# Kernel optimization log

Hardware: AMD Instinct MI355X
Metric: run time of the kernel (lower is better)

## Reference

```python
import jax, jax.numpy as jnp
import numpy as np

V = 32          # num_variables
T = 48          # num_time_bins
D = 512         # d_model
H = 8           # num_heads
HD = D // H     # head_dim = 64
OD = 16         # observation_dim
B = 4


def setup_inputs() -> dict:
    key = jax.random.key(0)
    ks = jax.random.split(key, 20)
    s = 0.02
    inp = {
        'h': jax.random.normal(ks[0], (B, T, V, D), jnp.float32),
        'observation_state': jax.random.normal(ks[1], (B, T, V, 2), jnp.float32),
        'Wq': jax.random.normal(ks[2], (D, D), jnp.float32) * s,
        'bq': jnp.zeros((D,), jnp.float32),
        'Wk': jax.random.normal(ks[3], (D, D), jnp.float32) * s,
        'bk': jnp.zeros((D,), jnp.float32),
        'Wv': jax.random.normal(ks[4], (D, D), jnp.float32) * s,
        'bv': jnp.zeros((D,), jnp.float32),
        'Wo': jax.random.normal(ks[5], (D, D), jnp.float32) * s,
        'bo': jnp.zeros((D,), jnp.float32),
        'Woq': jax.random.normal(ks[6], (2, H * OD), jnp.float32) * 0.5,
        'boq': jnp.zeros((H * OD,), jnp.float32),
        'Wok': jax.random.normal(ks[7], (2, H * OD), jnp.float32) * 0.5,
        'bok': jnp.zeros((H * OD,), jnp.float32),
        'variable_bias': jax.random.normal(ks[8], (H, V, V), jnp.float32) * 0.01,
        'relative_time_bias': jax.random.normal(ks[9], (H, 2 * T - 1), jnp.float32) * 0.01,
    }
    return inp


def reference(h, observation_state, Wq, bq, Wk, bk, Wv, bv, Wo, bo,
              Woq, boq, Wok, bok, variable_bias, relative_time_bias):
    N = T * V
    scale = 1.0 / np.sqrt(HD)
    obs_scale = 1.0 / np.sqrt(OD)

    # static index buffers (constants)
    flat_var_ids = jnp.tile(jnp.arange(V), T)                       # [N]
    flat_time_ids = jnp.repeat(jnp.arange(T), V)                    # [N]
    rel_index = flat_time_ids[:, None] - flat_time_ids[None, :] + (T - 1)  # [N,N]

    fh = h.reshape(B, N, D)
    fo = observation_state.reshape(B, N, 2)

    def heads(x, nh, hd):
        return x.reshape(B, N, nh, hd).transpose(0, 2, 1, 3)  # [B,H,N,hd]

    q = heads(fh @ Wq + bq, H, HD)
    k = heads(fh @ Wk + bk, H, HD)
    v = heads(fh @ Wv + bv, H, HD)
    oq = heads(fo @ Woq + boq, H, OD)
    ok = heads(fo @ Wok + bok, H, OD)

    content = jnp.einsum('bhnd,bhmd->bhnm', q, k) * scale
    obs = jnp.einsum('bhnd,bhmd->bhnm', oq, ok) * obs_scale
    var_scores = variable_bias[:, flat_var_ids[:, None], flat_var_ids[None, :]]  # [H,N,N]
    time_scores = relative_time_bias[:, rel_index]                                # [H,N,N]

    scores = content + obs + var_scores[None] + time_scores[None]
    attn = jax.nn.softmax(scores, axis=-1)  # dropout off (inference)
    out = jnp.einsum('bhnm,bhmd->bhnd', attn, v)
    out = out.transpose(0, 2, 1, 3).reshape(B, N, D)
    out = out @ Wo + bo
    return out.reshape(B, T, V, D)
```

## Files before the change

kernel.cpp:

```cpp
#include <hip/hip_runtime.h>
#include <math.h>

typedef __bf16 bf16x8 __attribute__((ext_vector_type(8)));
typedef float f32x4 __attribute__((ext_vector_type(4)));
typedef short short4v __attribute__((ext_vector_type(4)));
typedef short short8v __attribute__((ext_vector_type(8)));

#define NB 4
#define NT 48
#define NV 32
#define ND 512
#define NH 8
#define NN 1536
#define NBN 6144
#define L2E 1.44269504f

#define GLOAD_LDS(g, l) \
    __builtin_amdgcn_global_load_lds( \
        (const __attribute__((address_space(1))) void*)(g), \
        (__attribute__((address_space(3))) void*)(l), 16, 0, 0)

__global__ __launch_bounds__(256) void prep(
    const float* __restrict__ h, const float* __restrict__ obs,
    const float* __restrict__ Wq, const float* __restrict__ Wk,
    const float* __restrict__ Wv, const float* __restrict__ Wo,
    const float* __restrict__ bq, const float* __restrict__ bk,
    const float* __restrict__ bv,
    const float* __restrict__ Wok, const float* __restrict__ bok,
    __bf16* __restrict__ h_bf, __bf16* __restrict__ WcatT,
    __bf16* __restrict__ WoT, float* __restrict__ biascat,
    __bf16* __restrict__ kx)
{
    __shared__ float ts[64][68];
    const int tid = threadIdx.x;
    const int bx = blockIdx.x;
    if (bx < 1536) {
        int t = bx * 256 + tid;
        const float4* src = (const float4*)h + (size_t)t * 2;
        float4 a = src[0], b = src[1];
        __bf16 r[8] = {(__bf16)a.x, (__bf16)a.y, (__bf16)a.z, (__bf16)a.w,
                       (__bf16)b.x, (__bf16)b.y, (__bf16)b.z, (__bf16)b.w};
        *(uint4*)(h_bf + (size_t)t * 8) = *(uint4*)r;
    } else if (bx < 1792) {
        int bw = bx - 1536;
        const int p = bw >> 6, tile = bw & 63;
        const int k0 = (tile >> 3) * 64, c0 = (tile & 7) * 64;
        const float* W = (p == 0) ? Wq : (p == 1) ? Wk : (p == 2) ? Wv : Wo;
        const float scale = (p == 0) ? 0.125f * L2E : 1.0f;
        #pragma unroll
        for (int i = 0; i < 4; i++) {
            int r = (tid >> 4) + i * 16;
            float4 v = *(const float4*)(W + (size_t)(k0 + r) * 512 + c0 + (tid & 15) * 4);
            *(float4*)&ts[r][(tid & 15) * 4] = v;
        }
        __syncthreads();
        __bf16 tmp[16];
        #pragma unroll
        for (int j = 0; j < 16; j++)
            tmp[j] = (__bf16)(ts[(tid & 3) * 16 + j][tid >> 2] * scale);
        int crow = c0 + (tid >> 2);
        __bf16* dst = (p < 3)
            ? WcatT + ((size_t)(p * 512 + crow)) * 512 + k0 + (tid & 3) * 16
            : WoT   + ((size_t)crow) * 512 + k0 + (tid & 3) * 16;
        *(uint4*)dst = *(uint4*)tmp;
        *(uint4*)(dst + 8) = *(uint4*)(tmp + 8);
        if (p < 3 && k0 == 0 && tid < 64) {
            const float* bb = (p == 0) ? bq : (p == 1) ? bk : bv;
            biascat[p * 512 + c0 + tid] = bb[c0 + tid] * scale;
        }
    } else {
        int t = (bx - 1792) * 256 + tid;
        int row = t >> 1, half = t & 1;
        __bf16* dst = kx + (size_t)row * 96 + 64 + half * 16;
        if (half == 0) {
            int bh = row / NN, n = row - bh * NN;
            int b = bh >> 3, hh = bh & 7;
            size_t bn = (size_t)b * NN + n;
            float o0 = obs[bn * 2], o1 = obs[bn * 2 + 1];
            int f = hh * 16;
            __bf16 tmp[16];
            #pragma unroll
            for (int j = 0; j < 16; j++)
                tmp[j] = (__bf16)(o0 * Wok[f + j] + o1 * Wok[128 + f + j] + bok[f + j]);
            *(uint4*)dst       = *(uint4*)tmp;
            *(uint4*)(dst + 8) = *(uint4*)(tmp + 8);
        } else {
            uint4 z = {0, 0, 0, 0};
            *(uint4*)dst       = z;
            *(uint4*)(dst + 8) = z;
        }
    }
}

template<int TM, bool BF16OUT>
__global__ __launch_bounds__(256) void gemm_mfma(
    const __bf16* __restrict__ A, const __bf16* __restrict__ Bt,
    const float* __restrict__ bias, float* __restrict__ Cf,
    __bf16* __restrict__ qarr, __bf16* __restrict__ kx,
    __bf16* __restrict__ vt)
{
    constexpr int MT = TM / 32;
    __shared__ __align__(16) char smem[34816];
    char* const As0 = smem;
    char* const As1 = smem + TM * 64;
    char* const Bs0 = smem + TM * 128;
    char* const Bs1 = smem + TM * 128 + 8192;
    const int tid = threadIdx.x;
    const int w = tid >> 6, lane = tid & 63;
    const int quad = lane >> 4, l16 = lane & 15;
    const int wm = w >> 1, wn = w & 1;
    const int n0 = blockIdx.x * 128, m0 = blockIdx.y * TM;

    const int sm = tid >> 2;
    const int sk = ((tid & 3) ^ ((sm >> 1) & 3)) * 8;
    const __bf16* aptr = A  + (size_t)(m0 + sm) * 512 + sk;
    const __bf16* bptr = Bt + (size_t)(n0 + sm) * 512 + sk;

    f32x4 zero4 = {0.f, 0.f, 0.f, 0.f};
    f32x4 acc[MT][4];
    #pragma unroll
    for (int i = 0; i < MT; i++)
        #pragma unroll
        for (int j = 0; j < 4; j++) acc[i][j] = zero4;

    auto STAGE = [&](char* dA, char* dB, int kt) {
        GLOAD_LDS(aptr + kt, dA + tid * 16);
        if (TM == 128) GLOAD_LDS(aptr + 64 * 512 + kt, dA + 4096 + tid * 16);
        GLOAD_LDS(bptr + kt, dB + tid * 16);
        GLOAD_LDS(bptr + 64 * 512 + kt, dB + 4096 + tid * 16);
    };
    auto COMPUTE = [&](const char* Asb, const char* Bsb) {
        bf16x8 af[MT], bfr[4];
        #pragma unroll
        for (int mt = 0; mt < MT; mt++) {
            int rr = wm * (TM / 2) + mt * 16 + l16;
            af[mt] = *(const bf16x8*)(Asb + rr * 64 + (quad ^ ((rr >> 1) & 3)) * 16);
        }
        #pragma unroll
        for (int nt = 0; nt < 4; nt++) {
            int rr = wn * 64 + nt * 16 + l16;
            bfr[nt] = *(const bf16x8*)(Bsb + rr * 64 + (quad ^ ((rr >> 1) & 3)) * 16);
        }
        #pragma unroll
        for (int mt = 0; mt < MT; mt++)
            #pragma unroll
            for (int nt = 0; nt < 4; nt++)
                acc[mt][nt] = __builtin_amdgcn_mfma_f32_16x16x32_bf16(
                    af[mt], bfr[nt], acc[mt][nt], 0, 0, 0);
    };

    STAGE(As0, Bs0, 0);
    asm volatile("s_waitcnt vmcnt(0)" ::: "memory");
    __builtin_amdgcn_s_barrier();
    for (int kt = 0; kt < 512; kt += 64) {
        STAGE(As1, Bs1, kt + 32);
        COMPUTE(As0, Bs0);
        asm volatile("s_waitcnt vmcnt(0)" ::: "memory");
        __builtin_amdgcn_s_barrier();
        if (kt + 64 < 512) STAGE(As0, Bs0, kt + 64);
        COMPUTE(As1, Bs1);
        asm volatile("s_waitcnt vmcnt(0)" ::: "memory");
        __builtin_amdgcn_s_barrier();
    }

    __syncthreads();
    if (BF16OUT) {
        if (n0 >= 1024) {
            __bf16* CsT = (__bf16*)smem;
            #pragma unroll
            for (int nt = 0; nt < 4; nt++) {
                int cl = wn * 64 + nt * 16 + l16;
                float bia = bias[n0 + cl];
                #pragma unroll
                for (int mt = 0; mt < MT; mt++) {
                    int rl0 = wm * (TM / 2) + mt * 16 + quad * 4;
                    __bf16 pk[4];
                    #pragma unroll
                    for (int r = 0; r < 4; r++)
                        pk[r] = (__bf16)(acc[mt][nt][r] + bia);
                    *(uint2*)&CsT[cl * 136 + rl0] = *(uint2*)pk;
                }
            }
            __syncthreads();
            int cl = tid >> 1, half = tid & 1;
            int f0 = (n0 + cl) & 511;
            int hh = f0 >> 6, d = f0 & 63;
            int dt = d >> 4, l16v = d & 15;
            int bidx = m0 / NN, nm = m0 - bidx * NN;
            int bh = bidx * 8 + hh;
            int mtv = (nm >> 6) + half;
            #pragma unroll
            for (int j = 0; j < 8; j++) {
                uint4 v = *(uint4*)&CsT[cl * 136 + half * 64 + j * 8];
                __bf16* pp = (__bf16*)&v;
                int q0 = (j & 1) * 2;
                size_t fo = ((size_t)(bh * 24 + mtv) * 8 + (j >> 1) * 2 + (dt >> 1)) * 512
                            + (dt & 1) * 4 + l16v * 8;
                *(uint2*)(vt + fo + q0 * 128)       = *(uint2*)&pp[0];
                *(uint2*)(vt + fo + (q0 + 1) * 128) = *(uint2*)&pp[4];
            }
        } else {
            __bf16* Cs = (__bf16*)smem;
            #pragma unroll
            for (int mt = 0; mt < MT; mt++)
                #pragma unroll
                for (int nt = 0; nt < 4; nt++) {
                    int cl = wn * 64 + nt * 16 + l16;
                    float bia = bias[n0 + cl];
                    #pragma unroll
                    for (int r = 0; r < 4; r++) {
                        int rl = wm * (TM / 2) + mt * 16 + quad * 4 + r;
                        Cs[rl * 132 + cl] = (__bf16)(acc[mt][nt][r] + bia);
                    }
                }
            __syncthreads();
            int rl = tid >> 1, hb = tid & 1;
            int grow = m0 + rl;
            int col0 = n0 + hb * 64;
            int p = col0 >> 9, f0 = col0 & 511, hh = f0 >> 6;
            int bidx = grow / NN, n = grow - bidx * NN;
            __bf16* dst = (p == 0) ? qarr + (size_t)grow * 512 + f0
                                   : kx + ((size_t)(bidx * 8 + hh) * NN + n) * 96;
            #pragma unroll
            for (int j = 0; j < 8; j++) {
                uint2 lo = *(uint2*)&Cs[rl * 132 + hb * 64 + j * 8];
                uint2 hi = *(uint2*)&Cs[rl * 132 + hb * 64 + j * 8 + 4];
                uint4 v = {lo.x, lo.y, hi.x, hi.y};
                *(uint4*)(dst + j * 8) = v;
            }
        }
    } else {
        float* Csf = (float*)smem;
        #pragma unroll
        for (int mt = 0; mt < MT; mt++)
            #pragma unroll
            for (int nt = 0; nt < 4; nt++) {
                int cl = wn * 64 + nt * 16 + l16;
                float bia = bias[n0 + cl];
                #pragma unroll
                for (int r = 0; r < 4; r++) {
                    int rl = wm * (TM / 2) + mt * 16 + quad * 4 + r;
                    Csf[rl * 132 + cl] = acc[mt][nt][r] + bia;
                }
            }
        __syncthreads();
        int rl = tid >> 2, q4 = tid & 3;
        float* dst = Cf + (size_t)(m0 + rl) * 512 + n0 + q4 * 32;
        #pragma unroll
        for (int j = 0; j < 8; j++) {
            uint4 v = *(uint4*)&Csf[rl * 132 + q4 * 32 + j * 4];
            *(uint4*)(dst + j * 4) = v;
        }
    }
}

__global__ __launch_bounds__(256, 3) void attn_mfma(
    const __bf16* __restrict__ qarr, const __bf16* __restrict__ kx,
    const __bf16* __restrict__ vt, const float* __restrict__ obs,
    const float* __restrict__ Woq, const float* __restrict__ boq,
    const float* __restrict__ varb, const float* __restrict__ rtb,
    __bf16* __restrict__ aout)
{
    __shared__ __align__(16) __bf16 Ks[2][64][128];
    __shared__ float rts[96];

    const int tid = threadIdx.x;
    const int w = tid >> 6, lane = tid & 63;
    const int quad = lane >> 4, l16 = lane & 15;
    const int bh = blockIdx.x, qt = blockIdx.y;
    const int b = bh >> 3, h = bh & 7;
    const int n0 = qt * 64;

    if (tid < 95) rts[tid] = rtb[h * 95 + tid] * L2E;

    const int ck = (tid & 15) ^ ((tid >> 4) & 7);
    const __bf16* kbase = kx + (size_t)bh * NN * 96 + ck * 8;
    auto STAGE_K = [&](int p, int m0s) {
        #pragma unroll
        for (int i = 0; i < 4; i++) {
            int row = i * 16 + (tid >> 4);
            GLOAD_LDS(kbase + (size_t)(m0s + row) * 96,
                      (char*)Ks + p * 16384 + i * 4096 + tid * 16);
        }
    };
    STAGE_K(0, 0);
    STAGE_K(1, 64);

    const __bf16* vwb = vt + (size_t)bh * 24 * 4096 + lane * 8;

    const int nl = w * 16 + l16;
    const size_t qrow = (size_t)(b * NN + n0 + nl);
    bf16x8 bq_[3];
    bq_[0] = *(const bf16x8*)(qarr + qrow * 512 + h * 64 + quad * 8);
    bq_[1] = *(const bf16x8*)(qarr + qrow * 512 + h * 64 + 32 + quad * 8);
    {
        uint4 a2u = {0u, 0u, 0u, 0u};
        if (quad < 2) {
            float o0 = obs[qrow * 2], o1 = obs[qrow * 2 + 1];
            int f = h * 16 + quad * 8;
            const float sc = 0.25f * L2E;
            __bf16 tmp[8];
            #pragma unroll
            for (int j = 0; j < 8; j++)
                tmp[j] = (__bf16)(sc * (o0 * Woq[f + j] + o1 * Woq[128 + f + j]
                                        + boq[f + j]));
            a2u = *(uint4*)tmp;
        }
        bq_[2] = *(bf16x8*)&a2u;
    }

    const int rm = (w & 1) * 16 + l16;
    float4 vbA = *(const float4*)(varb + h * 1024 + rm * 32 + quad * 4);
    float4 vbB = *(const float4*)(varb + h * 1024 + rm * 32 + 16 + quad * 4);
    float vA[4] = {vbA.x * L2E, vbA.y * L2E, vbA.z * L2E, vbA.w * L2E};
    float vB[4] = {vbB.x * L2E, vbB.y * L2E, vbB.z * L2E, vbB.w * L2E};
    const int tn = 2 * qt + (w >> 1);

    union { __bf16 e[4]; short4v s; } one_u;
    #pragma unroll
    for (int j = 0; j < 4; j++) one_u.e[j] = (__bf16)1.0f;
    const short4v ones = one_u.s;

    f32x4 zero4 = {0.f, 0.f, 0.f, 0.f};
    f32x4 o_p[4];
    f32x4 lpa = zero4;
    #pragma unroll
    for (int i = 0; i < 4; i++) o_p[i] = zero4;

    auto QK = [&](int p, f32x4* sc) {
        __builtin_amdgcn_s_setprio(1);
        #pragma unroll
        for (int ct = 0; ct < 4; ct++) {
            f32x4 d = zero4;
            int row = ct * 16 + l16;
            #pragma unroll
            for (int ks = 0; ks < 3; ks++) {
                bf16x8 kf = *(const bf16x8*)((const char*)Ks + p * 16384
                                + row * 256 + (((ks * 4 + quad) ^ (row & 7)) * 16));
                d = __builtin_amdgcn_mfma_f32_16x16x32_bf16(kf, bq_[ks], d, 0, 0, 0);
            }
            sc[ct] = d;
        }
        __builtin_amdgcn_s_setprio(0);
    };
    auto SM = [&](const f32x4* sc, int mt, short4v* pf) {
        float tb0 = rts[tn - 2 * mt + 47];
        float tb1 = rts[tn - 2 * mt + 46];
        #pragma unroll
        for (int ct = 0; ct < 4; ct++) {
            float tb = (ct & 2) ? tb1 : tb0;
            const float* vv = (ct & 1) ? vB : vA;
            union { __bf16 e[4]; short4v s; } pk;
            #pragma unroll
            for (int r = 0; r < 4; r++)
                pk.e[r] = (__bf16)exp2f(sc[ct][r] + tb + vv[r]);
            pf[ct] = pk.s;
        }
    };
    auto PV = [&](const short8v* vfr, const short4v* pf) {
        __builtin_amdgcn_s_setprio(1);
        #pragma unroll
        for (int ct = 0; ct < 4; ct++) {
            lpa = __builtin_amdgcn_mfma_f32_16x16x16bf16_1k(ones, pf[ct], lpa, 0, 0, 0);
            #pragma unroll
            for (int dt = 0; dt < 4; dt++) {
                short8v v8 = vfr[ct * 2 + (dt >> 1)];
                short4v va = (dt & 1)
                    ? __builtin_shufflevector(v8, v8, 4, 5, 6, 7)
                    : __builtin_shufflevector(v8, v8, 0, 1, 2, 3);
                o_p[dt] = __builtin_amdgcn_mfma_f32_16x16x16bf16_1k(
                    va, pf[ct], o_p[dt], 0, 0, 0);
            }
        }
        __builtin_amdgcn_s_setprio(0);
    };

    __syncthreads();

    for (int i = 0; i < 12; i++) {
        const int mt0 = 2 * i;
        short8v v0[8];
        {
            const __bf16* vp = vwb + (size_t)mt0 * 4096;
            #pragma unroll
            for (int fi = 0; fi < 8; fi++)
                v0[fi] = *(const short8v*)(vp + fi * 512);
        }
        f32x4 sc0[4], sc1[4];
        QK(0, sc0);
        QK(1, sc1);
        __syncthreads();
        if (i < 11) {
            STAGE_K(0, (mt0 + 2) * 64);
            STAGE_K(1, (mt0 + 3) * 64);
        }
        short4v p0[4];
        SM(sc0, mt0, p0);
        short8v v1[8];
        {
            const __bf16* vp = vwb + (size_t)(mt0 + 1) * 4096;
            #pragma unroll
            for (int fi = 0; fi < 8; fi++)
                v1[fi] = *(const short8v*)(vp + fi * 512);
        }
        PV(v0, p0);
        short4v p1[4];
        SM(sc1, mt0 + 1, p1);
        PV(v1, p1);
        __syncthreads();
    }

    float linv = 1.0f / lpa[0];
    size_t abase = ((size_t)(b * NN) + n0 + nl) * 512 + h * 64 + quad * 4;
    #pragma unroll
    for (int dt = 0; dt < 4; dt++) {
        __bf16 ov[4];
        #pragma unroll
        for (int r = 0; r < 4; r++) ov[r] = (__bf16)(o_p[dt][r] * linv);
        *(uint2*)(aout + abase + dt * 16) = *(uint2*)ov;
    }
}

extern "C" void kernel_launch(void* const* d_in, const int* in_sizes, int n_in,
                              void* d_out, int out_size, void* d_ws, size_t ws_size,
                              hipStream_t stream)
{
    const float* h_   = (const float*)d_in[0];
    const float* obs  = (const float*)d_in[1];
    const float* Wq   = (const float*)d_in[2];
    const float* bq   = (const float*)d_in[3];
    const float* Wk   = (const float*)d_in[4];
    const float* bk   = (const float*)d_in[5];
    const float* Wv   = (const float*)d_in[6];
    const float* bv   = (const float*)d_in[7];
    const float* Wo   = (const float*)d_in[8];
    const float* bo   = (const float*)d_in[9];
    const float* Woq  = (const float*)d_in[10];
    const float* boq  = (const float*)d_in[11];
    const float* Wok  = (const float*)d_in[12];
    const float* bok  = (const float*)d_in[13];
    const float* varb = (const float*)d_in[14];
    const float* rtb  = (const float*)d_in[15];
    float* out = (float*)d_out;

    char* ws = (char*)d_ws;
    __bf16* h_bf    = (__bf16*)ws;                 ws += (size_t)NBN * 512 * 2;
    __bf16* qarr    = (__bf16*)ws;                 ws += (size_t)NBN * 512 * 2;
    __bf16* vt      = (__bf16*)ws;                 ws += (size_t)NBN * 512 * 2;
    __bf16* kx      = (__bf16*)ws;                 ws += ((size_t)32 * NN * 96 + 64) * 2;
    __bf16* attnout = (__bf16*)ws;                 ws += (size_t)NBN * 512 * 2;
    __bf16* WcatT   = (__bf16*)ws;                 ws += (size_t)1536 * 512 * 2;
    __bf16* WoT     = (__bf16*)ws;                 ws += (size_t)512 * 512 * 2;
    float*  biascat = (float*)ws;                  ws += 1536 * 4;

    prep<<<dim3(2176), dim3(256), 0, stream>>>(
        h_, obs, Wq, Wk, Wv, Wo, bq, bk, bv, Wok, bok,
        h_bf, WcatT, WoT, biascat, kx);
    gemm_mfma<128, true><<<dim3(12, 48), dim3(256), 0, stream>>>(
        h_bf, WcatT, biascat, nullptr, qarr, kx, vt);
    attn_mfma<<<dim3(32, 24), dim3(256), 0, stream>>>(qarr, kx, vt, obs, Woq, boq,
                                                      varb, rtb, attnout);
    gemm_mfma<64, false><<<dim3(4, 96), dim3(256), 0, stream>>>(
        attnout, WoT, bo, out, nullptr, nullptr, nullptr);
}
```

Baseline: 177.7 us.

## Split attention over key range with atomic partial accumulation and separate normalize pass

Splits each attention block's 24 key tiles into two halves via a third grid dimension. Each half accumulates unnormalized output and row sums into fp32 buffers with atomicAdd, and a new normalize kernel divides and converts to bf16. The K staging buffer shrinks to a single tile and the occupancy hint rises from 3 to 6 blocks, so there are twice as many blocks and more parallelism. The cost is zeroing a 12 MB fp32 buffer in prep, heavy atomic traffic, an extra kernel launch and pass, and a loss of double-buffering because K loads are now serialized per tile.

Measured after the change: 327.0 us. +84.0%, slower.

```diff
diff --git a/kernel.cpp b/kernel.cpp
--- a/kernel.cpp
+++ b/kernel.cpp
@@ -29,7 +29,8 @@
     const float* __restrict__ Wok, const float* __restrict__ bok,
     __bf16* __restrict__ h_bf, __bf16* __restrict__ WcatT,
     __bf16* __restrict__ WoT, float* __restrict__ biascat,
-    __bf16* __restrict__ kx)
+    __bf16* __restrict__ kx, float* __restrict__ oacc,
+    float* __restrict__ lpacc)
 {
     __shared__ float ts[64][68];
     const int tid = threadIdx.x;
@@ -68,7 +69,7 @@
             const float* bb = (p == 0) ? bq : (p == 1) ? bk : bv;
             biascat[p * 512 + c0 + tid] = bb[c0 + tid] * scale;
         }
-    } else {
+    } else if (bx < 2176) {
         int t = (bx - 1792) * 256 + tid;
         int row = t >> 1, half = t & 1;
         __bf16* dst = kx + (size_t)row * 96 + 64 + half * 16;
@@ -89,6 +90,14 @@
             *(uint4*)dst       = z;
             *(uint4*)(dst + 8) = z;
         }
+    } else if (bx < 5248) {
+        size_t t = (size_t)(bx - 2176) * 256 + tid;
+        uint4 z = {0, 0, 0, 0};
+        *(uint4*)(oacc + t * 4) = z;
+    } else {
+        size_t t = (size_t)(bx - 5248) * 256 + tid;
+        uint4 z = {0, 0, 0, 0};
+        *(uint4*)(lpacc + t * 4) = z;
     }
 }
 
@@ -254,37 +263,38 @@
     }
 }
 
-__global__ __launch_bounds__(256, 3) void attn_mfma(
+__global__ __launch_bounds__(256, 6) void attn_mfma(
     const __bf16* __restrict__ qarr, const __bf16* __restrict__ kx,
     const __bf16* __restrict__ vt, const float* __restrict__ obs,
     const float* __restrict__ Woq, const float* __restrict__ boq,
     const float* __restrict__ varb, const float* __restrict__ rtb,
-    __bf16* __restrict__ aout)
+    float* __restrict__ oacc, float* __restrict__ lpacc)
 {
-    __shared__ __align__(16) __bf16 Ks[2][64][128];
+    __shared__ __align__(16) __bf16 Ks[64][128];
     __shared__ float rts[96];
 
     const int tid = threadIdx.x;
     const int w = tid >> 6, lane = tid & 63;
     const int quad = lane >> 4, l16 = lane & 15;
     const int bh = blockIdx.x, qt = blockIdx.y;
+    const int z = blockIdx.z;
     const int b = bh >> 3, h = bh & 7;
     const int n0 = qt * 64;
+    const int mt0 = z * 12, mt1 = mt0 + 12;
 
     if (tid < 95) rts[tid] = rtb[h * 95 + tid] * L2E;
 
     const int ck = (tid & 15) ^ ((tid >> 4) & 7);
     const __bf16* kbase = kx + (size_t)bh * NN * 96 + ck * 8;
-    auto STAGE_K = [&](int p, int m0s) {
+    auto STAGE_K = [&](int m0s) {
         #pragma unroll
         for (int i = 0; i < 4; i++) {
             int row = i * 16 + (tid >> 4);
             GLOAD_LDS(kbase + (size_t)(m0s + row) * 96,
-                      (char*)Ks + p * 16384 + i * 4096 + tid * 16);
+                      (char*)Ks + i * 4096 + tid * 16);
         }
     };
-    STAGE_K(0, 0);
-    STAGE_K(1, 64);
+    STAGE_K(mt0 * 64);
 
     const __bf16* vwb = vt + (size_t)bh * 24 * 4096 + lane * 8;
 
@@ -327,7 +337,18 @@
     #pragma unroll
     for (int i = 0; i < 4; i++) o_p[i] = zero4;
 
-    auto QK = [&](int p, f32x4* sc) {
+    asm volatile("s_waitcnt vmcnt(0) lgkmcnt(0)" ::: "memory");
+    __builtin_amdgcn_s_barrier();
+
+    for (int mt = mt0; mt < mt1; mt++) {
+        short8v v0[8];
+        {
+            const __bf16* vp = vwb + (size_t)mt * 4096;
+            #pragma unroll
+            for (int fi = 0; fi < 8; fi++)
+                v0[fi] = *(const short8v*)(vp + fi * 512);
+        }
+        f32x4 sc[4];
         __builtin_amdgcn_s_setprio(1);
         #pragma unroll
         for (int ct = 0; ct < 4; ct++) {
@@ -335,17 +356,21 @@
             int row = ct * 16 + l16;
             #pragma unroll
             for (int ks = 0; ks < 3; ks++) {
-                bf16x8 kf = *(const bf16x8*)((const char*)Ks + p * 16384
-                                + row * 256 + (((ks * 4 + quad) ^ (row & 7)) * 16));
+                bf16x8 kf = *(const bf16x8*)((const char*)Ks + row * 256
+                                + (((ks * 4 + quad) ^ (row & 7)) * 16));
                 d = __builtin_amdgcn_mfma_f32_16x16x32_bf16(kf, bq_[ks], d, 0, 0, 0);
             }
             sc[ct] = d;
         }
         __builtin_amdgcn_s_setprio(0);
-    };
-    auto SM = [&](const f32x4* sc, int mt, short4v* pf) {
+
+        asm volatile("s_waitcnt lgkmcnt(0)" ::: "memory");
+        __builtin_amdgcn_s_barrier();
+        if (mt + 1 < mt1) STAGE_K((mt + 1) * 64);
+
         float tb0 = rts[tn - 2 * mt + 47];
         float tb1 = rts[tn - 2 * mt + 46];
+        short4v pf[4];
         #pragma unroll
         for (int ct = 0; ct < 4; ct++) {
             float tb = (ct & 2) ? tb1 : tb0;
@@ -356,15 +381,14 @@
                 pk.e[r] = (__bf16)exp2f(sc[ct][r] + tb + vv[r]);
             pf[ct] = pk.s;
         }
-    };
-    auto PV = [&](const short8v* vfr, const short4v* pf) {
+
         __builtin_amdgcn_s_setprio(1);
         #pragma unroll
         for (int ct = 0; ct < 4; ct++) {
             lpa = __builtin_amdgcn_mfma_f32_16x16x16bf16_1k(ones, pf[ct], lpa, 0, 0, 0);
             #pragma unroll
             for (int dt = 0; dt < 4; dt++) {
-                short8v v8 = vfr[ct * 2 + (dt >> 1)];
+                short8v v8 = v0[ct * 2 + (dt >> 1)];
                 short4v va = (dt & 1)
                     ? __builtin_shufflevector(v8, v8, 4, 5, 6, 7)
                     : __builtin_shufflevector(v8, v8, 0, 1, 2, 3);
@@ -373,52 +397,39 @@
             }
         }
         __builtin_amdgcn_s_setprio(0);
-    };
-
-    __syncthreads();
-
-    for (int i = 0; i < 12; i++) {
-        const int mt0 = 2 * i;
-        short8v v0[8];
-        {
-            const __bf16* vp = vwb + (size_t)mt0 * 4096;
-            #pragma unroll
-            for (int fi = 0; fi < 8; fi++)
-                v0[fi] = *(const short8v*)(vp + fi * 512);
-        }
-        f32x4 sc0[4], sc1[4];
-        QK(0, sc0);
-        QK(1, sc1);
-        __syncthreads();
-        if (i < 11) {
-            STAGE_K(0, (mt0 + 2) * 64);
-            STAGE_K(1, (mt0 + 3) * 64);
-        }
-        short4v p0[4];
-        SM(sc0, mt0, p0);
-        short8v v1[8];
-        {
-            const __bf16* vp = vwb + (size_t)(mt0 + 1) * 4096;
-            #pragma unroll
-            for (int fi = 0; fi < 8; fi++)
-                v1[fi] = *(const short8v*)(vp + fi * 512);
-        }
-        PV(v0, p0);
-        short4v p1[4];
-        SM(sc1, mt0 + 1, p1);
-        PV(v1, p1);
-        __syncthreads();
+
+        asm volatile("s_waitcnt vmcnt(0)" ::: "memory");
+        __builtin_amdgcn_s_barrier();
     }
 
-    float linv = 1.0f / lpa[0];
-    size_t abase = ((size_t)(b * NN) + n0 + nl) * 512 + h * 64 + quad * 4;
+    float* obase = oacc + ((size_t)(b * NN) + n0 + nl) * 512 + h * 64 + quad * 4;
     #pragma unroll
-    for (int dt = 0; dt < 4; dt++) {
-        __bf16 ov[4];
-        #pragma unroll
-        for (int r = 0; r < 4; r++) ov[r] = (__bf16)(o_p[dt][r] * linv);
-        *(uint2*)(aout + abase + dt * 16) = *(uint2*)ov;
-    }
+    for (int dt = 0; dt < 4; dt++)
+        #pragma unroll
+        for (int r = 0; r < 4; r++)
+            atomicAdd(obase + dt * 16 + r, o_p[dt][r]);
+    if (quad == 0)
+        atomicAdd(lpacc + (size_t)bh * NN + n0 + nl, lpa[0]);
+}
+
+__global__ __launch_bounds__(256) void norm_attn(
+    const float* __restrict__ oacc, const float* __restrict__ lpacc,
+    __bf16* __restrict__ aout)
+{
+    size_t t = (size_t)blockIdx.x * 256 + threadIdx.x;
+    size_t e = t * 8;
+    int bn = (int)(e >> 9);
+    int col = (int)(e & 511);
+    int b = bn / NN, n = bn - b * NN;
+    int h = col >> 6;
+    float linv = 1.0f / lpacc[(size_t)(b * 8 + h) * NN + n];
+    float4 x0 = *(const float4*)(oacc + e);
+    float4 x1 = *(const float4*)(oacc + e + 4);
+    __bf16 ov[8] = {(__bf16)(x0.x * linv), (__bf16)(x0.y * linv),
+                    (__bf16)(x0.z * linv), (__bf16)(x0.w * linv),
+                    (__bf16)(x1.x * linv), (__bf16)(x1.y * linv),
+                    (__bf16)(x1.z * linv), (__bf16)(x1.w * linv)};
+    *(uint4*)(aout + e) = *(uint4*)ov;
 }
 
 extern "C" void kernel_launch(void* const* d_in, const int* in_sizes, int n_in,
@@ -452,14 +463,18 @@
     __bf16* WcatT   = (__bf16*)ws;                 ws += (size_t)1536 * 512 * 2;
     __bf16* WoT     = (__bf16*)ws;                 ws += (size_t)512 * 512 * 2;
     float*  biascat = (float*)ws;                  ws += 1536 * 4;
-
-    prep<<<dim3(2176), dim3(256), 0, stream>>>(
+    float*  oacc    = (float*)ws;                  ws += (size_t)NBN * 512 * 4;
+    float*  lpacc   = (float*)ws;                  ws += (size_t)32 * NN * 4;
+
+    prep<<<dim3(5296), dim3(256), 0, stream>>>(
         h_, obs, Wq, Wk, Wv, Wo, bq, bk, bv, Wok, bok,
-        h_bf, WcatT, WoT, biascat, kx);
+        h_bf, WcatT, WoT, biascat, kx, oacc, lpacc);
     gemm_mfma<128, true><<<dim3(12, 48), dim3(256), 0, stream>>>(
         h_bf, WcatT, biascat, nullptr, qarr, kx, vt);
-    attn_mfma<<<dim3(32, 24), dim3(256), 0, stream>>>(qarr, kx, vt, obs, Woq, boq,
-                                                      varb, rtb, attnout);
+    attn_mfma<<<dim3(32, 24, 2), dim3(256), 0, stream>>>(qarr, kx, vt, obs,
+                                                         Woq, boq, varb, rtb,
+                                                         oacc, lpacc);
+    norm_attn<<<dim3(1536), dim3(256), 0, stream>>>(oacc, lpacc, attnout);
     gemm_mfma<64, false><<<dim3(4, 96), dim3(256), 0, stream>>>(
         attnout, WoT, bo, out, nullptr, nullptr, nullptr);
 }
```
